# Kernel tuning notes

Hardware: AMD Instinct MI355X
Metric: run time of the kernel (lower is better)

## Reference

```python
import jax, jax.numpy as jnp
import numpy as np

NUM_BINS = 5
TAIL = 1.0
MIN_BIN_W = 1e-3
MIN_BIN_H = 1e-3


def conv2d(x, w, b, pad):
    y = jax.lax.conv_general_dilated(x, w, (1, 1), [(pad, pad), (pad, pad)],
                                     dimension_numbers=("NCHW", "OIHW", "NCHW"))
    return y + b[None, :, None, None]


def transform_net(x, w1, b1, w2, b2, w3, b3):
    h = jax.nn.relu(conv2d(x, w1, b1, 1))
    h = jax.nn.relu(conv2d(h, w2, b2, 0))
    return conv2d(h, w3, b3, 1)


def _pad_last_left(a):
    return jnp.pad(a, [(0, 0)] * (a.ndim - 1) + [(1, 0)])


def quadratic_spline(x, uw, uh):
    # nflows quadratic_spline with left=bottom=-TAIL, right=top=TAIL
    inputs = (x + TAIL) / (2.0 * TAIL)  # rescale to [0,1]
    widths = jax.nn.softmax(uw, axis=-1)
    widths = MIN_BIN_W + (1.0 - MIN_BIN_W * NUM_BINS) * widths
    uh_exp = jnp.exp(uh)  # [..., NUM_BINS-1]
    first_w = 0.5 * widths[..., 0]
    last_w = 0.5 * widths[..., -1]
    numerator = (0.5 * first_w * uh_exp[..., 0] + 0.5 * last_w * uh_exp[..., -1]
                 + jnp.sum(0.5 * (uh_exp[..., :-1] + uh_exp[..., 1:]) * widths[..., 1:-1], axis=-1))
    constant = numerator / (1.0 - 0.5 * first_w - 0.5 * last_w)
    uh_exp = jnp.concatenate([constant[..., None], uh_exp, constant[..., None]], axis=-1)  # NUM_BINS+1 knot heights
    area = jnp.sum(0.5 * (uh_exp[..., :-1] + uh_exp[..., 1:]) * widths, axis=-1, keepdims=True)
    heights = uh_exp / area
    heights = MIN_BIN_H + (1.0 - MIN_BIN_H) * heights
    bin_cdf = jnp.cumsum(0.5 * (heights[..., :-1] + heights[..., 1:]) * widths, axis=-1)
    bin_cdf = _pad_last_left(bin_cdf.at[..., -1].set(1.0))  # [..., NUM_BINS+1]
    bin_loc = jnp.cumsum(widths, axis=-1)
    bin_loc = _pad_last_left(bin_loc.at[..., -1].set(1.0))  # [..., NUM_BINS+1]
    # searchsorted: bin index per element
    idx = jnp.clip(jnp.sum((inputs[..., None] >= bin_loc).astype(jnp.int32), axis=-1) - 1, 0, NUM_BINS - 1)
    take = lambda t, i: jnp.take_along_axis(t, i[..., None], axis=-1)[..., 0]
    loc = take(bin_loc, idx)
    cdf = take(bin_cdf, idx)
    h_l = take(heights, idx)
    h_r = take(heights, idx + 1)
    w = take(widths, idx)
    alpha = (inputs - loc) / w
    a = 0.5 * (h_r - h_l) * w
    b = h_l * w
    out = jnp.clip(a * alpha * alpha + b * alpha + cdf, 0.0, 1.0)
    lad = jnp.log(alpha * (h_r - h_l) + h_l)  # log(top-bottom)-log(right-left)=0
    out = out * (2.0 * TAIL) - TAIL
    return out, lad


def unconstrained_quadratic_spline(x, uw, uh):
    inside = (x >= -TAIL) & (x <= TAIL)
    xc = jnp.clip(x, -TAIL, TAIL)
    s_out, s_lad = quadratic_spline(xc, uw, uh)
    out = jnp.where(inside, s_out, x)  # linear tails
    lad = jnp.where(inside, s_lad, 0.0)
    return out, lad


def setup_inputs() -> dict:
    key = jax.random.key(0)
    ks = jax.random.split(key, 8)
    B, C, H, W = 32, 12, 128, 128
    hid = 128
    c_half = C // 2
    c_out = c_half * (2 * NUM_BINS - 1)  # 54
    s = 0.05
    return {
        "x": jax.random.normal(ks[0], (B, C, H, W), dtype=jnp.float32),
        "objective": jnp.zeros((B,), dtype=jnp.float32),
        "w1": s * jax.random.normal(ks[1], (hid, c_half, 3, 3), dtype=jnp.float32),
        "b1": jnp.zeros((hid,), dtype=jnp.float32),
        "w2": s * jax.random.normal(ks[2], (hid, hid, 1, 1), dtype=jnp.float32),
        "b2": jnp.zeros((hid,), dtype=jnp.float32),
        "w3": s * jax.random.normal(ks[3], (c_out, hid, 3, 3), dtype=jnp.float32),
        "b3": jnp.zeros((c_out,), dtype=jnp.float32),
    }


def reference(x, objective, w1, b1, w2, b2, w3, b3):
    identity_split, transform_split = jnp.split(x, 2, axis=1)
    params = transform_net(identity_split, w1, b1, w2, b2, w3, b3)  # [B, c/2*(2K-1), H, W]
    b, c, h, w = transform_split.shape
    params = params.reshape(b, c, -1, h, w).transpose(0, 1, 3, 4, 2)  # [B,c,H,W,2K-1]
    uw = params[..., :NUM_BINS]
    uh = params[..., NUM_BINS:]
    transformed, lad = unconstrained_quadratic_spline(transform_split, uw, uh)
    output = jnp.concatenate([identity_split, transformed], axis=1)
    objective = objective + jnp.sum(lad, axis=(1, 2, 3))
    return output, objective
```

## Files before the change

### kernel.cpp

```cpp
#include <hip/hip_runtime.h>
#include <hip/hip_bf16.h>
#include <math.h>

#define B 32
#define CFULL 12
#define CH 6
#define HH 128
#define WW 128
#define HID 128
#define CO3 54
#define NB 5
#define OUT_ELEMS (B*CFULL*HH*WW)
#define H2_BYTES (size_t)(B*HH*WW*HID*2)
#define WFRAG_ELEMS (9*4*4*64*8)
#define W1F_ELEMS (2*8*64*8)
#define W2F_ELEMS (4*8*64*8)

typedef __bf16 bf16x8 __attribute__((ext_vector_type(8)));
typedef float f32x4 __attribute__((ext_vector_type(4)));

__device__ __forceinline__ ushort f2bf(float f) {
    uint b = __float_as_uint(f);
    uint r = (b + 0x7FFFu + ((b >> 16) & 1u)) >> 16;
    return (ushort)r;
}

union UBF { uint4 u; bf16x8 b; };

__global__ __launch_bounds__(256) void k_prep_all(
    const float* __restrict__ w1, const float* __restrict__ w2, const float* __restrict__ w3,
    const float* __restrict__ obj_in, float* __restrict__ obj_out,
    ushort* __restrict__ W1f, ushort* __restrict__ W2f, ushort* __restrict__ W3f)
{
    int idx = blockIdx.x * 256 + threadIdx.x;
    if (blockIdx.x == 0 && threadIdx.x < B) obj_out[threadIdx.x] = obj_in[threadIdx.x];

    if (idx < WFRAG_ELEMS) {
        int j    = idx & 7;
        int lane = (idx >> 3) & 63;
        int nf   = (idx >> 9) & 3;
        int kb   = (idx >> 11) & 3;
        int t    = idx >> 13;
        int co = nf * 16 + (lane & 15);
        int ci = kb * 32 + 8 * (lane >> 4) + j;
        float v = (co < CO3) ? w3[(co * HID + ci) * 9 + t] : 0.f;
        W3f[idx] = f2bf(v);
    } else if (idx < WFRAG_ELEMS + W1F_ELEMS) {
        int i1 = idx - WFRAG_ELEMS;
        int j = i1 & 7, lane = (i1 >> 3) & 63, nf = (i1 >> 9) & 7, ks = i1 >> 12;
        int co = nf * 16 + (lane & 15);
        int k  = ks * 32 + (lane >> 4) * 8 + j;
        W1f[i1] = f2bf(k < 54 ? w1[co * 54 + k] : 0.f);
    } else if (idx < WFRAG_ELEMS + W1F_ELEMS + W2F_ELEMS) {
        int i2 = idx - WFRAG_ELEMS - W1F_ELEMS;
        int j = i2 & 7, lane = (i2 >> 3) & 63, nf = (i2 >> 9) & 7, ks = (i2 >> 12) & 3;
        int co = nf * 16 + (lane & 15);
        int ci = ks * 32 + (lane >> 4) * 8 + j;
        W2f[i2] = f2bf(w2[co * 128 + ci]);
    }
}

__global__ __launch_bounds__(256) void k_conv12(
    const float* __restrict__ x,
    const ushort* __restrict__ W1f, const float* __restrict__ b1,
    const ushort* __restrict__ W2f, const float* __restrict__ b2,
    ushort* __restrict__ h2)
{
    __shared__ char buf1[21248];
    __shared__ char buf2[32768];

    ushort* xs = (ushort*)buf1;
    char* Albase = buf1 + 4864;
    char* h1 = buf2;
    char* h2st = buf2;

    const int b = blockIdx.x >> 7;
    const int h = blockIdx.x & 127;
    const int tid = threadIdx.x;
    const int lane = tid & 63;
    const int wv = tid >> 6;
    const int lr = lane & 15;
    const int kg = lane >> 4;

    for (int i = tid; i < 6*3*130; i += 256) {
        int ci = i / 390; int rem = i - ci*390;
        int r = rem / 130; int xw = rem - r*130;
        int hh = h + r - 1, ww = xw - 1;
        float v = 0.f;
        if (hh >= 0 && hh < HH && ww >= 0 && ww < WW)
            v = x[((b*CFULL + ci)*HH + hh)*WW + ww];
        xs[(ci*3 + r)*132 + xw] = f2bf(v);
    }
    __syncthreads();

    for (int it = 0; it < 4; ++it) {
        int item = (it << 8) + tid;
        int px = item & 127;
        int g  = item >> 7;
        uint pk[4];
#pragma unroll
        for (int jj = 0; jj < 4; ++jj) {
            int k0 = g*8 + jj*2;
            int k1 = k0 + 1;
            uint v0 = 0, v1 = 0;
            if (k0 < 54) { int ci = k0/9; int rem = k0 - ci*9; int r = rem/3; int dx = rem - r*3;
                           v0 = xs[(ci*3 + r)*132 + px + dx]; }
            if (k1 < 54) { int ci = k1/9; int rem = k1 - ci*9; int r = rem/3; int dx = rem - r*3;
                           v1 = xs[(ci*3 + r)*132 + px + dx]; }
            pk[jj] = v0 | (v1 << 16);
        }
        uint4 q; q.x = pk[0]; q.y = pk[1]; q.z = pk[2]; q.w = pk[3];
        *(uint4*)(Albase + px*128 + ((g << 4) ^ (((px >> 1) & 7) << 4))) = q;
    }
    __syncthreads();

    f32x4 acc[2][8];
#pragma unroll
    for (int mm = 0; mm < 2; ++mm)
#pragma unroll
        for (int nf = 0; nf < 8; ++nf) acc[mm][nf] = (f32x4){0.f,0.f,0.f,0.f};

    const int px0 = wv*32 + lr;
    const int px1 = px0 + 16;
#pragma unroll
    for (int ks = 0; ks < 2; ++ks) {
        UBF a0, a1;
        a0.u = *(const uint4*)(Albase + px0*128 + ((ks*64 + kg*16) ^ (((px0 >> 1) & 7) << 4)));
        a1.u = *(const uint4*)(Albase + px1*128 + ((ks*64 + kg*16) ^ (((px1 >> 1) & 7) << 4)));
        const char* wp = (const char*)W1f + ks*8192 + lane*16;
#pragma unroll
        for (int nf = 0; nf < 8; ++nf) {
            UBF bf; bf.u = *(const uint4*)(wp + nf*1024);
            acc[0][nf] = __builtin_amdgcn_mfma_f32_16x16x32_bf16(a0.b, bf.b, acc[0][nf], 0, 0, 0);
            acc[1][nf] = __builtin_amdgcn_mfma_f32_16x16x32_bf16(a1.b, bf.b, acc[1][nf], 0, 0, 0);
        }
    }

    float b1v[8];
#pragma unroll
    for (int nf = 0; nf < 8; ++nf) b1v[nf] = b1[nf*16 + lr];
#pragma unroll
    for (int mm = 0; mm < 2; ++mm)
#pragma unroll
        for (int nf = 0; nf < 8; ++nf) {
            int co2 = (nf*16 + lr) * 2;
#pragma unroll
            for (int rg = 0; rg < 4; ++rg) {
                int px = wv*32 + mm*16 + kg*4 + rg;
                float v = fmaxf(acc[mm][nf][rg] + b1v[nf], 0.f);
                *(ushort*)(h1 + px*256 + (co2 ^ (((px >> 1) & 7) << 4))) = f2bf(v);
            }
        }
    __syncthreads();

#pragma unroll
    for (int mm = 0; mm < 2; ++mm)
#pragma unroll
        for (int nf = 0; nf < 8; ++nf) acc[mm][nf] = (f32x4){0.f,0.f,0.f,0.f};
#pragma unroll
    for (int ks = 0; ks < 4; ++ks) {
        UBF a0, a1;
        a0.u = *(const uint4*)(h1 + px0*256 + ((ks*64 + kg*16) ^ (((px0 >> 1) & 7) << 4)));
        a1.u = *(const uint4*)(h1 + px1*256 + ((ks*64 + kg*16) ^ (((px1 >> 1) & 7) << 4)));
        const char* wp = (const char*)W2f + ks*8192 + lane*16;
#pragma unroll
        for (int nf = 0; nf < 8; ++nf) {
            UBF bf; bf.u = *(const uint4*)(wp + nf*1024);
            acc[0][nf] = __builtin_amdgcn_mfma_f32_16x16x32_bf16(a0.b, bf.b, acc[0][nf], 0, 0, 0);
            acc[1][nf] = __builtin_amdgcn_mfma_f32_16x16x32_bf16(a1.b, bf.b, acc[1][nf], 0, 0, 0);
        }
    }

    __syncthreads();

    float b2v[8];
#pragma unroll
    for (int nf = 0; nf < 8; ++nf) b2v[nf] = b2[nf*16 + lr];
#pragma unroll
    for (int mm = 0; mm < 2; ++mm)
#pragma unroll
        for (int nf = 0; nf < 8; ++nf) {
            int co2 = (nf*16 + lr) * 2;
#pragma unroll
            for (int rg = 0; rg < 4; ++rg) {
                int px = wv*32 + mm*16 + kg*4 + rg;
                float v = fmaxf(acc[mm][nf][rg] + b2v[nf], 0.f);
                *(ushort*)(h2st + px*256 + (co2 ^ (((px >> 1) & 7) << 4))) = f2bf(v);
            }
        }
    __syncthreads();

    const size_t outbase = (size_t)((b*HH + h)*WW) * HID;
    for (int c = tid; c < 2048; c += 256) {
        int px = c >> 4; int cb = (c & 15) << 4;
        uint4 v = *(const uint4*)(h2st + px*256 + (cb ^ (((px >> 1) & 7) << 4)));
        *(uint4*)&h2[outbase + (size_t)c*8] = v;
    }
}

__global__ __launch_bounds__(256, 3) void k_conv3_spline(
    const float* __restrict__ x,
    const ushort* __restrict__ h2,
    const ushort* __restrict__ Wfrag, const float* __restrict__ b3,
    float* __restrict__ out, float* __restrict__ obj)
{
    __shared__ char xsb[33792];
    __shared__ float red[4];

    const int g = blockIdx.x;
    const int b = blockIdx.y;
    const int tid = threadIdx.x;
    const int px = tid & 127;
    const int t7 = (tid >> 7) & 1;

    float xr0, xr1, xr2, xr3, xr4, xr5;
    {
        size_t base;
#define PRO(RR, KS, DST) \
        base = ((size_t)(b*CFULL + (t7 + 2*(KS)))*HH + (2*g + (RR)))*WW + px; \
        out[base] = x[base]; \
        DST = x[base + (size_t)CH*HH*WW];
        PRO(0,0,xr0) PRO(0,1,xr1) PRO(0,2,xr2)
        PRO(1,0,xr3) PRO(1,1,xr4) PRO(1,2,xr5)
#undef PRO
    }

    const int lane = tid & 63;
    const int wv   = tid >> 6;
    const int mrow = wv >> 1;
    const int ncol = wv & 1;
    const int kg   = lane >> 4;
    const int lr   = lane & 15;

    f32x4 acc[8][2];
#pragma unroll
    for (int mf = 0; mf < 8; ++mf) {
        acc[mf][0] = (f32x4){0.f,0.f,0.f,0.f};
        acc[mf][1] = (f32x4){0.f,0.f,0.f,0.f};
    }

    const char* wbase = (const char*)Wfrag + ncol*2048 + lane*16;

#pragma unroll 1
    for (int q = 0; q < 4; ++q) {
        if (q) __syncthreads();

        for (int i = tid; i < 2080; i += 256) {
            int r = i / 520; int rem = i - r*520;
            int wl = rem >> 2; int c4 = rem & 3;
            int hh = 2*g - 1 + r, ww = wl - 1;
            uint4 v = {0,0,0,0};
            if (hh >= 0 && hh < HH && ww >= 0 && ww < WW)
                v = *(const uint4*)&h2[(size_t)((b*HH + hh)*WW + ww)*HID + q*32 + c4*8];
            *(uint4*)(xsb + r*8448 + wl*64 + ((c4*16) ^ ((wl & 3) << 4))) = v;
        }
        __syncthreads();

#pragma unroll 1
        for (int r3 = 0; r3 < 3; ++r3) {
            const char* rowb = xsb + (mrow + r3)*8448;
#pragma unroll
            for (int dx = 0; dx < 3; ++dx) {
                const int t = r3*3 + dx;
                const char* wp = wbase + (((t << 2) + q) << 12);
                UBF b0; b0.u = *(const uint4*)(wp);
                UBF b1; b1.u = *(const uint4*)(wp + 1024);
#pragma unroll
                for (int mf = 0; mf < 8; ++mf) {
                    const int wl = mf*16 + lr + dx;
                    UBF a; a.u = *(const uint4*)(rowb + wl*64 + ((kg*16) ^ ((wl & 3) << 4)));
                    acc[mf][0] = __builtin_amdgcn_mfma_f32_16x16x32_bf16(a.b, b0.b, acc[mf][0], 0, 0, 0);
                    acc[mf][1] = __builtin_amdgcn_mfma_f32_16x16x32_bf16(a.b, b1.b, acc[mf][1], 0, 0, 0);
                }
            }
        }
    }
    __syncthreads();

    float* pl = (float*)xsb;
    float lad = 0.f;

#pragma unroll
    for (int r = 0; r < 2; ++r) {
        if (r) __syncthreads();

        if (mrow == r) {
#pragma unroll
            for (int mf = 0; mf < 8; ++mf)
#pragma unroll
                for (int nf = 0; nf < 2; ++nf) {
                    const int co = ncol*32 + nf*16 + lr;
                    const int p0 = mf*16 + (kg << 2);
                    *(f32x4*)&pl[co*132 + p0] = acc[mf][nf];
                }
        }
        __syncthreads();

#pragma unroll
        for (int ks = 0; ks < 3; ++ks) {
            const int c = __builtin_amdgcn_readfirstlane(t7 + 2*ks);
            const float xraw = (r == 0) ? (ks == 0 ? xr0 : ks == 1 ? xr1 : xr2)
                                        : (ks == 0 ? xr3 : ks == 1 ? xr4 : xr5);

            float u[9];
#pragma unroll
            for (int j = 0; j < 9; ++j) u[j] = pl[(c*9 + j)*132 + px] + b3[c*9 + j];

            bool inside = (xraw >= -1.f) && (xraw <= 1.f);
            float xc = fminf(fmaxf(xraw, -1.f), 1.f);
            float in01 = (xc + 1.f) * 0.5f;

            float m = u[0];
#pragma unroll
            for (int i2 = 1; i2 < 5; ++i2) m = fmaxf(m, u[i2]);
            float e[5], es = 0.f;
#pragma unroll
            for (int i2 = 0; i2 < 5; ++i2) { e[i2] = expf(u[i2] - m); es += e[i2]; }
            float wdt[5];
#pragma unroll
            for (int i2 = 0; i2 < 5; ++i2) wdt[i2] = 0.001f + (1.f - 0.001f*NB) * (e[i2] / es);

            float eh[4];
#pragma unroll
            for (int i2 = 0; i2 < 4; ++i2) eh[i2] = expf(u[5 + i2]);

            float first_w = 0.5f * wdt[0], last_w = 0.5f * wdt[4];
            float numer = 0.5f*first_w*eh[0] + 0.5f*last_w*eh[3]
                        + 0.5f*(eh[0]+eh[1])*wdt[1]
                        + 0.5f*(eh[1]+eh[2])*wdt[2]
                        + 0.5f*(eh[2]+eh[3])*wdt[3];
            float cst = numer / (1.f - 0.5f*first_w - 0.5f*last_w);

            float kn[6] = {cst, eh[0], eh[1], eh[2], eh[3], cst};
            float area = 0.f;
#pragma unroll
            for (int i2 = 0; i2 < 5; ++i2) area += 0.5f*(kn[i2]+kn[i2+1])*wdt[i2];
            float hts[6];
#pragma unroll
            for (int i2 = 0; i2 < 6; ++i2) hts[i2] = 0.001f + (1.f - 0.001f) * (kn[i2] / area);

            float C[6]; C[0] = 0.f;
#pragma unroll
            for (int i2 = 0; i2 < 5; ++i2) C[i2+1] = C[i2] + 0.5f*(hts[i2]+hts[i2+1])*wdt[i2];
            C[5] = 1.f;
            float L[6]; L[0] = 0.f;
#pragma unroll
            for (int i2 = 0; i2 < 5; ++i2) L[i2+1] = L[i2] + wdt[i2];
            L[5] = 1.f;

            int idx = 0;
#pragma unroll
            for (int i2 = 1; i2 < 6; ++i2) idx += (in01 >= L[i2]) ? 1 : 0;
            idx = min(idx, 4);

            float loc = L[0], cdf = C[0], hl = hts[0], hr = hts[1], wb2 = wdt[0];
#pragma unroll
            for (int i2 = 1; i2 < 5; ++i2) {
                if (i2 == idx) { loc = L[i2]; cdf = C[i2]; hl = hts[i2]; hr = hts[i2+1]; wb2 = wdt[i2]; }
            }

            float alpha = (in01 - loc) / wb2;
            float aa = 0.5f*(hr - hl)*wb2;
            float bb = hl*wb2;
            float o = fminf(fmaxf(aa*alpha*alpha + bb*alpha + cdf, 0.f), 1.f);
            float sl = logf(alpha*(hr - hl) + hl);
            float outv = o*2.f - 1.f;
            if (!inside) { outv = xraw; sl = 0.f; }
            out[((size_t)(b*CFULL + CH + c)*HH + (2*g + r))*WW + px] = outv;
            lad += sl;
        }
    }

#pragma unroll
    for (int off = 32; off > 0; off >>= 1) lad += __shfl_down(lad, off, 64);
    if ((tid & 63) == 0) red[tid >> 6] = lad;
    __syncthreads();
    if (tid == 0) {
        float s = red[0] + red[1] + red[2] + red[3];
        atomicAdd(&obj[b], s);
    }
}

extern "C" void kernel_launch(void* const* d_in, const int* in_sizes, int n_in,
                              void* d_out, int out_size, void* d_ws, size_t ws_size,
                              hipStream_t stream) {
    const float* x   = (const float*)d_in[0];
    const float* obj = (const float*)d_in[1];
    const float* w1  = (const float*)d_in[2];
    const float* b1  = (const float*)d_in[3];
    const float* w2  = (const float*)d_in[4];
    const float* b2  = (const float*)d_in[5];
    const float* w3  = (const float*)d_in[6];
    const float* b3  = (const float*)d_in[7];

    float* out_t = (float*)d_out;
    float* obj_o = out_t + OUT_ELEMS;
    ushort* h2  = (ushort*)d_ws;
    ushort* W3f = (ushort*)((char*)d_ws + H2_BYTES);
    ushort* W1f = (ushort*)((char*)d_ws + H2_BYTES + 147456);
    ushort* W2f = (ushort*)((char*)d_ws + H2_BYTES + 147456 + 16384);

    const int prep_items = WFRAG_ELEMS + W1F_ELEMS + W2F_ELEMS;
    k_prep_all<<<(prep_items + 255)/256, 256, 0, stream>>>(w1, w2, w3, obj, obj_o, W1f, W2f, W3f);
    k_conv12<<<B*HH, 256, 0, stream>>>(x, W1f, b1, W2f, b2, h2);
    k_conv3_spline<<<dim3(HH/2, B), 256, 0, stream>>>(x, h2, W3f, b3, out_t, obj_o);
}
```

Baseline: 295.3 us.

## Process four output rows per conv3 block and shrink conv12 LDS footprint

The conv3+spline kernel now uses 512-thread blocks that each produce four image rows instead of two. The 6-row h2 halo is staged once and shared by more output rows, which cuts redundant halo loads, and the LDS swizzle pattern changes. The conv12 kernel merges its two shared buffers into one 32KB buffer, with an extra barrier, and declares higher occupancy via launch bounds. The risks are larger LDS per conv3 block limiting residency, and half the threads sitting idle in the second spline channel pass.

```diff
diff --git a/kernel.cpp b/kernel.cpp
--- a/kernel.cpp
+++ b/kernel.cpp
@@ -60,19 +60,18 @@
     }
 }
 
-__global__ __launch_bounds__(256) void k_conv12(
+__global__ __launch_bounds__(256, 5) void k_conv12(
     const float* __restrict__ x,
     const ushort* __restrict__ W1f, const float* __restrict__ b1,
     const ushort* __restrict__ W2f, const float* __restrict__ b2,
     ushort* __restrict__ h2)
 {
-    __shared__ char buf1[21248];
-    __shared__ char buf2[32768];
-
-    ushort* xs = (ushort*)buf1;
-    char* Albase = buf1 + 4864;
-    char* h1 = buf2;
-    char* h2st = buf2;
+    __shared__ char buf[32768];
+
+    ushort* xs = (ushort*)buf;
+    char* Albase = buf + 4864;
+    char* h1 = buf;
+    char* h2st = buf;
 
     const int b = blockIdx.x >> 7;
     const int h = blockIdx.x & 127;
@@ -135,6 +134,7 @@
             acc[1][nf] = __builtin_amdgcn_mfma_f32_16x16x32_bf16(a1.b, bf.b, acc[1][nf], 0, 0, 0);
         }
     }
+    __syncthreads();
 
     float b1v[8];
 #pragma unroll
@@ -170,7 +170,6 @@
             acc[1][nf] = __builtin_amdgcn_mfma_f32_16x16x32_bf16(a1.b, bf.b, acc[1][nf], 0, 0, 0);
         }
     }
-
     __syncthreads();
 
     float b2v[8];
@@ -198,31 +197,33 @@
     }
 }
 
-__global__ __launch_bounds__(256, 3) void k_conv3_spline(
+__global__ __launch_bounds__(512, 6) void k_conv3_spline(
     const float* __restrict__ x,
     const ushort* __restrict__ h2,
     const ushort* __restrict__ Wfrag, const float* __restrict__ b3,
     float* __restrict__ out, float* __restrict__ obj)
 {
-    __shared__ char xsb[33792];
-    __shared__ float red[4];
+    __shared__ char xsb[50688];
+    __shared__ float red[8];
 
     const int g = blockIdx.x;
     const int b = blockIdx.y;
     const int tid = threadIdx.x;
     const int px = tid & 127;
-    const int t7 = (tid >> 7) & 1;
-
-    float xr0, xr1, xr2, xr3, xr4, xr5;
-    {
-        size_t base;
-#define PRO(RR, KS, DST) \
-        base = ((size_t)(b*CFULL + (t7 + 2*(KS)))*HH + (2*g + (RR)))*WW + px; \
-        out[base] = x[base]; \
-        DST = x[base + (size_t)CH*HH*WW];
-        PRO(0,0,xr0) PRO(0,1,xr1) PRO(0,2,xr2)
-        PRO(1,0,xr3) PRO(1,1,xr4) PRO(1,2,xr5)
-#undef PRO
+    const int t7 = tid >> 7;
+
+    float xr[4][2];
+#pragma unroll
+    for (int r = 0; r < 4; ++r) {
+        const size_t base = ((size_t)(b*CFULL + t7)*HH + (4*g + r))*WW + px;
+        out[base] = x[base];
+        xr[r][0] = x[base + (size_t)CH*HH*WW];
+        xr[r][1] = 0.f;
+        if (tid < 256) {
+            const size_t base2 = ((size_t)(b*CFULL + 4 + t7)*HH + (4*g + r))*WW + px;
+            out[base2] = x[base2];
+            xr[r][1] = x[base2 + (size_t)CH*HH*WW];
+        }
     }
 
     const int lane = tid & 63;
@@ -245,14 +246,14 @@
     for (int q = 0; q < 4; ++q) {
         if (q) __syncthreads();
 
-        for (int i = tid; i < 2080; i += 256) {
+        for (int i = tid; i < 3120; i += 512) {
             int r = i / 520; int rem = i - r*520;
             int wl = rem >> 2; int c4 = rem & 3;
-            int hh = 2*g - 1 + r, ww = wl - 1;
+            int hh = 4*g - 1 + r, ww = wl - 1;
             uint4 v = {0,0,0,0};
             if (hh >= 0 && hh < HH && ww >= 0 && ww < WW)
                 v = *(const uint4*)&h2[(size_t)((b*HH + hh)*WW + ww)*HID + q*32 + c4*8];
-            *(uint4*)(xsb + r*8448 + wl*64 + ((c4*16) ^ ((wl & 3) << 4))) = v;
+            *(uint4*)(xsb + r*8448 + wl*64 + ((c4*16) ^ (((wl >> 1) & 3) << 4))) = v;
         }
         __syncthreads();
 
@@ -268,7 +269,7 @@
 #pragma unroll
                 for (int mf = 0; mf < 8; ++mf) {
                     const int wl = mf*16 + lr + dx;
-                    UBF a; a.u = *(const uint4*)(rowb + wl*64 + ((kg*16) ^ ((wl & 3) << 4)));
+                    UBF a; a.u = *(const uint4*)(rowb + wl*64 + ((kg*16) ^ (((wl >> 1) & 3) << 4)));
                     acc[mf][0] = __builtin_amdgcn_mfma_f32_16x16x32_bf16(a.b, b0.b, acc[mf][0], 0, 0, 0);
                     acc[mf][1] = __builtin_amdgcn_mfma_f32_16x16x32_bf16(a.b, b1.b, acc[mf][1], 0, 0, 0);
                 }
@@ -281,7 +282,7 @@
     float lad = 0.f;
 
 #pragma unroll
-    for (int r = 0; r < 2; ++r) {
+    for (int r = 0; r < 4; ++r) {
         if (r) __syncthreads();
 
         if (mrow == r) {
@@ -297,77 +298,78 @@
         __syncthreads();
 
 #pragma unroll
-        for (int ks = 0; ks < 3; ++ks) {
-            const int c = __builtin_amdgcn_readfirstlane(t7 + 2*ks);
-            const float xraw = (r == 0) ? (ks == 0 ? xr0 : ks == 1 ? xr1 : xr2)
-                                        : (ks == 0 ? xr3 : ks == 1 ? xr4 : xr5);
-
-            float u[9];
-#pragma unroll
-            for (int j = 0; j < 9; ++j) u[j] = pl[(c*9 + j)*132 + px] + b3[c*9 + j];
-
-            bool inside = (xraw >= -1.f) && (xraw <= 1.f);
-            float xc = fminf(fmaxf(xraw, -1.f), 1.f);
-            float in01 = (xc + 1.f) * 0.5f;
-
-            float m = u[0];
-#pragma unroll
-            for (int i2 = 1; i2 < 5; ++i2) m = fmaxf(m, u[i2]);
-            float e[5], es = 0.f;
-#pragma unroll
-            for (int i2 = 0; i2 < 5; ++i2) { e[i2] = expf(u[i2] - m); es += e[i2]; }
-            float wdt[5];
-#pragma unroll
-            for (int i2 = 0; i2 < 5; ++i2) wdt[i2] = 0.001f + (1.f - 0.001f*NB) * (e[i2] / es);
-
-            float eh[4];
-#pragma unroll
-            for (int i2 = 0; i2 < 4; ++i2) eh[i2] = expf(u[5 + i2]);
-
-            float first_w = 0.5f * wdt[0], last_w = 0.5f * wdt[4];
-            float numer = 0.5f*first_w*eh[0] + 0.5f*last_w*eh[3]
-                        + 0.5f*(eh[0]+eh[1])*wdt[1]
-                        + 0.5f*(eh[1]+eh[2])*wdt[2]
-                        + 0.5f*(eh[2]+eh[3])*wdt[3];
-            float cst = numer / (1.f - 0.5f*first_w - 0.5f*last_w);
-
-            float kn[6] = {cst, eh[0], eh[1], eh[2], eh[3], cst};
-            float area = 0.f;
-#pragma unroll
-            for (int i2 = 0; i2 < 5; ++i2) area += 0.5f*(kn[i2]+kn[i2+1])*wdt[i2];
-            float hts[6];
-#pragma unroll
-            for (int i2 = 0; i2 < 6; ++i2) hts[i2] = 0.001f + (1.f - 0.001f) * (kn[i2] / area);
-
-            float C[6]; C[0] = 0.f;
-#pragma unroll
-            for (int i2 = 0; i2 < 5; ++i2) C[i2+1] = C[i2] + 0.5f*(hts[i2]+hts[i2+1])*wdt[i2];
-            C[5] = 1.f;
-            float L[6]; L[0] = 0.f;
-#pragma unroll
-            for (int i2 = 0; i2 < 5; ++i2) L[i2+1] = L[i2] + wdt[i2];
-            L[5] = 1.f;
-
-            int idx = 0;
-#pragma unroll
-            for (int i2 = 1; i2 < 6; ++i2) idx += (in01 >= L[i2]) ? 1 : 0;
-            idx = min(idx, 4);
-
-            float loc = L[0], cdf = C[0], hl = hts[0], hr = hts[1], wb2 = wdt[0];
-#pragma unroll
-            for (int i2 = 1; i2 < 5; ++i2) {
-                if (i2 == idx) { loc = L[i2]; cdf = C[i2]; hl = hts[i2]; hr = hts[i2+1]; wb2 = wdt[i2]; }
+        for (int s = 0; s < 2; ++s) {
+            if (s == 0 || tid < 256) {
+                const int c = __builtin_amdgcn_readfirstlane(s ? 4 + t7 : t7);
+                const float xraw = xr[r][s];
+
+                float u[9];
+#pragma unroll
+                for (int j = 0; j < 9; ++j) u[j] = pl[(c*9 + j)*132 + px] + b3[c*9 + j];
+
+                bool inside = (xraw >= -1.f) && (xraw <= 1.f);
+                float xc = fminf(fmaxf(xraw, -1.f), 1.f);
+                float in01 = (xc + 1.f) * 0.5f;
+
+                float m = u[0];
+#pragma unroll
+                for (int i2 = 1; i2 < 5; ++i2) m = fmaxf(m, u[i2]);
+                float e[5], es = 0.f;
+#pragma unroll
+                for (int i2 = 0; i2 < 5; ++i2) { e[i2] = expf(u[i2] - m); es += e[i2]; }
+                float wdt[5];
+#pragma unroll
+                for (int i2 = 0; i2 < 5; ++i2) wdt[i2] = 0.001f + (1.f - 0.001f*NB) * (e[i2] / es);
+
+                float eh[4];
+#pragma unroll
+                for (int i2 = 0; i2 < 4; ++i2) eh[i2] = expf(u[5 + i2]);
+
+                float first_w = 0.5f * wdt[0], last_w = 0.5f * wdt[4];
+                float numer = 0.5f*first_w*eh[0] + 0.5f*last_w*eh[3]
+                            + 0.5f*(eh[0]+eh[1])*wdt[1]
+                            + 0.5f*(eh[1]+eh[2])*wdt[2]
+                            + 0.5f*(eh[2]+eh[3])*wdt[3];
+                float cst = numer / (1.f - 0.5f*first_w - 0.5f*last_w);
+
+                float kn[6] = {cst, eh[0], eh[1], eh[2], eh[3], cst};
+                float area = 0.f;
+#pragma unroll
+                for (int i2 = 0; i2 < 5; ++i2) area += 0.5f*(kn[i2]+kn[i2+1])*wdt[i2];
+                float hts[6];
+#pragma unroll
+                for (int i2 = 0; i2 < 6; ++i2) hts[i2] = 0.001f + (1.f - 0.001f) * (kn[i2] / area);
+
+                float C[6]; C[0] = 0.f;
+#pragma unroll
+                for (int i2 = 0; i2 < 5; ++i2) C[i2+1] = C[i2] + 0.5f*(hts[i2]+hts[i2+1])*wdt[i2];
+                C[5] = 1.f;
+                float L[6]; L[0] = 0.f;
+#pragma unroll
+                for (int i2 = 0; i2 < 5; ++i2) L[i2+1] = L[i2] + wdt[i2];
+                L[5] = 1.f;
+
+                int idx = 0;
+#pragma unroll
+                for (int i2 = 1; i2 < 6; ++i2) idx += (in01 >= L[i2]) ? 1 : 0;
+                idx = min(idx, 4);
+
+                float loc = L[0], cdf = C[0], hl = hts[0], hr = hts[1], wb2 = wdt[0];
+#pragma unroll
+                for (int i2 = 1; i2 < 5; ++i2) {
+                    if (i2 == idx) { loc = L[i2]; cdf = C[i2]; hl = hts[i2]; hr = hts[i2+1]; wb2 = wdt[i2]; }
+                }
+
+                float alpha = (in01 - loc) / wb2;
+                float aa = 0.5f*(hr - hl)*wb2;
+                float bb = hl*wb2;
+                float o = fminf(fmaxf(aa*alpha*alpha + bb*alpha + cdf, 0.f), 1.f);
+                float sl = logf(alpha*(hr - hl) + hl);
+                float outv = o*2.f - 1.f;
+                if (!inside) { outv = xraw; sl = 0.f; }
+                out[((size_t)(b*CFULL + CH + c)*HH + (4*g + r))*WW + px] = outv;
+                lad += sl;
             }
-
-            float alpha = (in01 - loc) / wb2;
-            float aa = 0.5f*(hr - hl)*wb2;
-            float bb = hl*wb2;
-            float o = fminf(fmaxf(aa*alpha*alpha + bb*alpha + cdf, 0.f), 1.f);
-            float sl = logf(alpha*(hr - hl) + hl);
-            float outv = o*2.f - 1.f;
-            if (!inside) { outv = xraw; sl = 0.f; }
-            out[((size_t)(b*CFULL + CH + c)*HH + (2*g + r))*WW + px] = outv;
-            lad += sl;
         }
     }
 
@@ -376,7 +378,9 @@
     if ((tid & 63) == 0) red[tid >> 6] = lad;
     __syncthreads();
     if (tid == 0) {
-        float s = red[0] + red[1] + red[2] + red[3];
+        float s = 0.f;
+#pragma unroll
+        for (int i = 0; i < 8; ++i) s += red[i];
         atomicAdd(&obj[b], s);
     }
 }
@@ -403,5 +407,5 @@
     const int prep_items = WFRAG_ELEMS + W1F_ELEMS + W2F_ELEMS;
     k_prep_all<<<(prep_items + 255)/256, 256, 0, stream>>>(w1, w2, w3, obj, obj_o, W1f, W2f, W3f);
     k_conv12<<<B*HH, 256, 0, stream>>>(x, W1f, b1, W2f, b2, h2);
-    k_conv3_spline<<<dim3(HH/2, B), 256, 0, stream>>>(x, h2, W3f, b3, out_t, obj_o);
+    k_conv3_spline<<<dim3(HH/4, B), 512, 0, stream>>>(x, h2, W3f, b3, out_t, obj_o);
 }
```

Result: slower. 903.2 us (+205.9%).
